# Kernel optimization log

Measured on AMD Instinct MI355X. Metric: run time of the kernel, lower is better.

Reference implementation:

```python
import jax, jax.numpy as jnp
from jax import lax
import numpy as np

STRIDE = 8  # == slice_width
EMBED_DIM = 512


def setup_inputs() -> dict:
    key = jax.random.key(0)
    k0, k1, k2, k3, k4 = jax.random.split(key, 5)
    B, C, H, W = 64, 1, 32, 8192
    images = jax.random.normal(k0, (B, C, H, W), dtype=jnp.float32)
    u = lambda k, s: jax.random.uniform(k, s, jnp.float32, -0.08, 0.08)
    conv_w = u(k1, (1, 1, 3, 3))            # OIHW, 1->1 channel, 3x3
    conv_b = u(k2, (1,))
    lin_w = u(k3, (H * STRIDE, EMBED_DIM))   # bridge: slice_height*slice_width -> embed_dim
    lin_b = u(k4, (EMBED_DIM,))
    return {"images": images, "conv_w": conv_w, "conv_b": conv_b, "lin_w": lin_w, "lin_b": lin_b}


def reference(images, conv_w, conv_b, lin_w, lin_b):
    B, C, H, W = images.shape
    S = W // STRIDE  # src_len (number of width-slices)
    # Windowing: non-overlapping width slices -> a single reshape/transpose
    # [B, C, H, W] -> [B*S, C, H, stride]
    sl = images.reshape(B, C, H, S, STRIDE).transpose(0, 3, 1, 2, 4)
    pixels = sl.reshape(B * S, C, H, STRIDE)
    # Conv2d(1,1,3x3, padding=1) + ReLU (same spatial shape)
    y = lax.conv_general_dilated(
        pixels, conv_w, window_strides=(1, 1), padding="SAME",
        dimension_numbers=("NCHW", "OIHW", "NCHW"))
    y = jax.nn.relu(y + conv_b[None, :, None, None])
    # Bridge linear on flattened slice pixels
    feats = y.reshape(B * S, H * STRIDE)
    emb = feats @ lin_w + lin_b
    return emb.reshape(B, S, EMBED_DIM)
```

## Files before the change

### kernel.cpp

```cpp
#include <hip/hip_runtime.h>
#include <hip/hip_bf16.h>
#include <stdint.h>

#define HEIGHT 32
#define WIDTH  8192
#define KDIM   256
#define NDIM   512
#define NSLICES 65536
#define NMTILES 2048

typedef float f32x4  __attribute__((ext_vector_type(4)));
typedef float f32x16 __attribute__((ext_vector_type(16)));
typedef short bf16x8 __attribute__((ext_vector_type(8)));

__device__ __forceinline__ ushort f2bf(float x) {
  union { float f; uint32_t u; } un; un.f = x;
  uint32_t u = un.u;
  u += 0x7FFFu + ((u >> 16) & 1u);
  return (ushort)(u >> 16);
}

__device__ __forceinline__ void load_row8(float* r, const float* p) {
  f32x4 lo = *reinterpret_cast<const f32x4*>(p);
  f32x4 hi = *reinterpret_cast<const f32x4*>(p + 4);
#pragma unroll
  for (int w = 0; w < 4; ++w) { r[w] = lo[w]; r[4 + w] = hi[w]; }
}

__global__ __launch_bounds__(256) void prep_wt2_kernel(const float* __restrict__ lin_w,
                                                       ushort* __restrict__ wt2) {
  const int idx = blockIdx.x * 256 + threadIdx.x;
  const int ln  = idx & 63;
  const int k0  = (idx >> 6) & 15;
  const int nb  = idx >> 10;
  const int n   = nb * 32 + (ln & 31);
  const int kb  = k0 * 16 + (ln >> 5) * 8;
  bf16x8 p;
#pragma unroll
  for (int e = 0; e < 8; ++e) p[e] = (short)f2bf(lin_w[(size_t)(kb + e) * NDIM + n]);
  *reinterpret_cast<bf16x8*>(wt2 + (size_t)idx * 8) = p;
}

__global__ __launch_bounds__(256) void fused_kernel(
    const float* __restrict__ images, const float* __restrict__ conv_w,
    const float* __restrict__ conv_b, const ushort* __restrict__ wt2,
    const float* __restrict__ lin_b, float* __restrict__ out) {
  __shared__ ushort A[16 * 64 * 8];

  const int tid = threadIdx.x;
  const int blk = blockIdx.x;

  float cw[9];
#pragma unroll
  for (int i = 0; i < 9; ++i) cw[i] = conv_w[i];
  const float cb = conv_b[0];

  {
    const int sl = tid & 31;
    const int q  = tid >> 5;
    const int s  = blk * 32 + sl;
    const int b  = s >> 10;
    const int slb = s & 1023;
    const float* base = images + (size_t)b * (HEIGHT * WIDTH) + (size_t)slb * 8;
    const int h0 = q * 4;

    float pr[8], cu[8], nx[8];
    if (h0 > 0) load_row8(pr, base + (size_t)(h0 - 1) * WIDTH);
    else {
#pragma unroll
      for (int w = 0; w < 8; ++w) pr[w] = 0.f;
    }
    load_row8(cu, base + (size_t)h0 * WIDTH);

#pragma unroll
    for (int i = 0; i < 4; ++i) {
      const int h = h0 + i;
      if (h + 1 < HEIGHT) load_row8(nx, base + (size_t)(h + 1) * WIDTH);
      else {
#pragma unroll
        for (int w = 0; w < 8; ++w) nx[w] = 0.f;
      }
      float y[8];
#pragma unroll
      for (int w = 0; w < 8; ++w) y[w] = cb;
#pragma unroll
      for (int dw = 0; dw < 3; ++dw) {
        const float c0 = cw[dw], c1 = cw[3 + dw], c2 = cw[6 + dw];
#pragma unroll
        for (int w = 0; w < 8; ++w) {
          const int iw = w + dw - 1;
          if (iw >= 0 && iw < 8) {
            y[w] = fmaf(pr[iw], c0, y[w]);
            y[w] = fmaf(cu[iw], c1, y[w]);
            y[w] = fmaf(nx[iw], c2, y[w]);
          }
        }
      }
      bf16x8 pack;
#pragma unroll
      for (int w = 0; w < 8; ++w) pack[w] = (short)f2bf(fmaxf(y[w], 0.f));
      const int ln = ((h & 1) << 5) | sl;
      const int k0 = h >> 1;
      *reinterpret_cast<bf16x8*>(A + ((size_t)k0 * 64 + ln) * 8) = pack;
#pragma unroll
      for (int w = 0; w < 8; ++w) { pr[w] = cu[w]; cu[w] = nx[w]; }
    }
  }
  __syncthreads();

  const int lane = tid & 63;
  const int wv   = tid >> 6;
  const int la   = lane & 31;
  const int lb   = lane >> 5;
  const size_t row0 = (size_t)blk * 32;

  const ushort* abase = A + (size_t)lane * 8;

#pragma unroll
  for (int pass = 0; pass < 2; ++pass) {
    const int nfb = wv * 4 + pass * 2;
    const ushort* bb = wt2 + ((size_t)nfb * 16) * 512 + (size_t)lane * 8;

    f32x16 acc0, acc1;
#pragma unroll
    for (int i = 0; i < 16; ++i) { acc0[i] = 0.f; acc1[i] = 0.f; }

#pragma unroll
    for (int k0 = 0; k0 < 16; ++k0) {
      const bf16x8 af  = *reinterpret_cast<const bf16x8*>(abase + (size_t)k0 * 512);
      const bf16x8 bf0 = *reinterpret_cast<const bf16x8*>(bb + (size_t)k0 * 512);
      const bf16x8 bf1 = *reinterpret_cast<const bf16x8*>(bb + (size_t)(16 + k0) * 512);
      acc0 = __builtin_amdgcn_mfma_f32_32x32x16_bf16(af, bf0, acc0, 0, 0, 0);
      acc1 = __builtin_amdgcn_mfma_f32_32x32x16_bf16(af, bf1, acc1, 0, 0, 0);
    }

#pragma unroll
    for (int nf = 0; nf < 2; ++nf) {
      const int col = (nfb + nf) * 32 + la;
      const float bias = lin_b[col];
      const f32x16& a = nf ? acc1 : acc0;
#pragma unroll
      for (int reg = 0; reg < 16; ++reg) {
        const int rr = (reg & 3) + 8 * (reg >> 2) + 4 * lb;
        out[(row0 + rr) * NDIM + col] = a[reg] + bias;
      }
    }
  }
}

extern "C" void kernel_launch(void* const* d_in, const int* in_sizes, int n_in,
                              void* d_out, int out_size, void* d_ws, size_t ws_size,
                              hipStream_t stream) {
  const float* images = (const float*)d_in[0];
  const float* conv_w = (const float*)d_in[1];
  const float* conv_b = (const float*)d_in[2];
  const float* lin_w  = (const float*)d_in[3];
  const float* lin_b  = (const float*)d_in[4];
  float* out = (float*)d_out;
  ushort* wt2 = (ushort*)d_ws;

  hipLaunchKernelGGL(prep_wt2_kernel, dim3(64), dim3(256), 0, stream, lin_w, wt2);
  hipLaunchKernelGGL(fused_kernel, dim3(NMTILES), dim3(256), 0, stream,
                     images, conv_w, conv_b, wt2, lin_b, out);
}
```

Measured before the change: 55.61 us.

## Stream weight fragments into double-buffered LDS via global_load_lds pipeline

Replaces direct global loads of weight fragments with asynchronous global-to-LDS copies, double-buffered across the K loop, and merges the two N passes into one pass with four accumulators per wave. The aim is to hide global load latency of B behind MFMAs and let each A fragment be read once per k step instead of twice. It adds 32 KB of LDS per block, which may lower occupancy, raises register use with four 16-wide accumulators, and uses hand-placed waitcnts that could be fragile.

```diff
diff --git a/kernel.cpp b/kernel.cpp
--- a/kernel.cpp
+++ b/kernel.cpp
@@ -12,6 +12,11 @@
 typedef float f32x4  __attribute__((ext_vector_type(4)));
 typedef float f32x16 __attribute__((ext_vector_type(16)));
 typedef short bf16x8 __attribute__((ext_vector_type(8)));
+
+#define GLOAD_LDS16(g, l)                                                       \
+  __builtin_amdgcn_global_load_lds(                                             \
+      (const __attribute__((address_space(1))) void*)(g),                       \
+      (__attribute__((address_space(3))) void*)(l), 16, 0, 0)
 
 __device__ __forceinline__ ushort f2bf(float x) {
   union { float f; uint32_t u; } un; un.f = x;
@@ -46,6 +51,7 @@
     const float* __restrict__ conv_b, const ushort* __restrict__ wt2,
     const float* __restrict__ lin_b, float* __restrict__ out) {
   __shared__ ushort A[16 * 64 * 8];
+  __shared__ ushort Bb[2][16][512];
 
   const int tid = threadIdx.x;
   const int blk = blockIdx.x;
@@ -112,38 +118,59 @@
   const int wv   = tid >> 6;
   const int la   = lane & 31;
   const int lb   = lane >> 5;
-  const size_t row0 = (size_t)blk * 32;
+
+  const ushort* bsrc = wt2 + (size_t)lane * 8;
+#define BFRAG_SRC(nf, k) (bsrc + (((wv * 4 + (nf)) * 16 + (k)) * 512))
+
+#pragma unroll
+  for (int nf = 0; nf < 4; ++nf)
+    GLOAD_LDS16(BFRAG_SRC(nf, 0), &Bb[0][wv * 4 + nf][0]);
+
+  f32x16 acc[4];
+#pragma unroll
+  for (int nf = 0; nf < 4; ++nf)
+#pragma unroll
+    for (int i = 0; i < 16; ++i) acc[nf][i] = 0.f;
 
   const ushort* abase = A + (size_t)lane * 8;
 
 #pragma unroll
-  for (int pass = 0; pass < 2; ++pass) {
-    const int nfb = wv * 4 + pass * 2;
-    const ushort* bb = wt2 + ((size_t)nfb * 16) * 512 + (size_t)lane * 8;
-
-    f32x16 acc0, acc1;
+  for (int k0 = 0; k0 < 16; ++k0) {
+    const int cur = k0 & 1;
+    if (k0 < 15) {
+      asm volatile("s_waitcnt lgkmcnt(0)" ::: "memory");
+      __builtin_amdgcn_sched_barrier(0);
+      const int nxt = cur ^ 1;
 #pragma unroll
-    for (int i = 0; i < 16; ++i) { acc0[i] = 0.f; acc1[i] = 0.f; }
-
-#pragma unroll
-    for (int k0 = 0; k0 < 16; ++k0) {
-      const bf16x8 af  = *reinterpret_cast<const bf16x8*>(abase + (size_t)k0 * 512);
-      const bf16x8 bf0 = *reinterpret_cast<const bf16x8*>(bb + (size_t)k0 * 512);
-      const bf16x8 bf1 = *reinterpret_cast<const bf16x8*>(bb + (size_t)(16 + k0) * 512);
-      acc0 = __builtin_amdgcn_mfma_f32_32x32x16_bf16(af, bf0, acc0, 0, 0, 0);
-      acc1 = __builtin_amdgcn_mfma_f32_32x32x16_bf16(af, bf1, acc1, 0, 0, 0);
+      for (int nf = 0; nf < 4; ++nf)
+        GLOAD_LDS16(BFRAG_SRC(nf, k0 + 1), &Bb[nxt][wv * 4 + nf][0]);
+      asm volatile("s_waitcnt vmcnt(4)" ::: "memory");
+      __builtin_amdgcn_sched_barrier(0);
+    } else {
+      asm volatile("s_waitcnt vmcnt(0)" ::: "memory");
+      __builtin_amdgcn_sched_barrier(0);
     }
 
+    const bf16x8 af = *reinterpret_cast<const bf16x8*>(abase + (size_t)k0 * 512);
+    const bf16x8 b0 = *reinterpret_cast<const bf16x8*>(&Bb[cur][wv * 4 + 0][0] + (size_t)lane * 8);
+    const bf16x8 b1 = *reinterpret_cast<const bf16x8*>(&Bb[cur][wv * 4 + 1][0] + (size_t)lane * 8);
+    const bf16x8 b2 = *reinterpret_cast<const bf16x8*>(&Bb[cur][wv * 4 + 2][0] + (size_t)lane * 8);
+    const bf16x8 b3 = *reinterpret_cast<const bf16x8*>(&Bb[cur][wv * 4 + 3][0] + (size_t)lane * 8);
+    acc[0] = __builtin_amdgcn_mfma_f32_32x32x16_bf16(af, b0, acc[0], 0, 0, 0);
+    acc[1] = __builtin_amdgcn_mfma_f32_32x32x16_bf16(af, b1, acc[1], 0, 0, 0);
+    acc[2] = __builtin_amdgcn_mfma_f32_32x32x16_bf16(af, b2, acc[2], 0, 0, 0);
+    acc[3] = __builtin_amdgcn_mfma_f32_32x32x16_bf16(af, b3, acc[3], 0, 0, 0);
+  }
+
+  const size_t row0 = (size_t)blk * 32;
 #pragma unroll
-    for (int nf = 0; nf < 2; ++nf) {
-      const int col = (nfb + nf) * 32 + la;
-      const float bias = lin_b[col];
-      const f32x16& a = nf ? acc1 : acc0;
+  for (int nf = 0; nf < 4; ++nf) {
+    const int col = wv * 128 + nf * 32 + la;
+    const float bias = lin_b[col];
 #pragma unroll
-      for (int reg = 0; reg < 16; ++reg) {
-        const int rr = (reg & 3) + 8 * (reg >> 2) + 4 * lb;
-        out[(row0 + rr) * NDIM + col] = a[reg] + bias;
-      }
+    for (int reg = 0; reg < 16; ++reg) {
+      const int rr = (reg & 3) + 8 * (reg >> 2) + 4 * lb;
+      out[(row0 + rr) * NDIM + col] = acc[nf][reg] + bias;
     }
   }
 }
```

After: 57.20 us. 2.9% more time.

## Split fused conv+GEMM into separate conv and register-resident-weight GEMM kernels

Applied to the files above, without the earlier changes.

Splits the fused kernel in two. A conv kernel writes bf16 features in MFMA-ready layout to workspace, and a GEMM kernel keeps a 32-column weight fragment in registers while looping over 8 row tiles. This lets each weight fragment be reused across many rows instead of reloading it per block. The cost is an extra global round trip of 32 MB of bf16 features plus a second launch, and the new path runs only when the workspace is large enough.

```diff
diff --git a/kernel.cpp b/kernel.cpp
--- a/kernel.cpp
+++ b/kernel.cpp
@@ -8,6 +8,8 @@
 #define NDIM   512
 #define NSLICES 65536
 #define NMTILES 2048
+#define WT_BYTES (NDIM * KDIM * 2)
+#define FEATS_BYTES ((size_t)NSLICES * KDIM * 2)
 
 typedef float f32x4  __attribute__((ext_vector_type(4)));
 typedef float f32x16 __attribute__((ext_vector_type(16)));
@@ -41,12 +43,119 @@
   *reinterpret_cast<bf16x8*>(wt2 + (size_t)idx * 8) = p;
 }
 
+__global__ __launch_bounds__(256) void conv_kernel(
+    const float* __restrict__ images, const float* __restrict__ conv_w,
+    const float* __restrict__ conv_b, ushort* __restrict__ feats2) {
+  const int blk = blockIdx.x;
+  const int tid = threadIdx.x;
+
+  float cw[9];
+#pragma unroll
+  for (int i = 0; i < 9; ++i) cw[i] = conv_w[i];
+  const float cb = conv_b[0];
+
+  const int sl = tid & 31;
+  const int q  = tid >> 5;
+  const int s  = blk * 32 + sl;
+  const int b  = s >> 10;
+  const int slb = s & 1023;
+  const float* base = images + (size_t)b * (HEIGHT * WIDTH) + (size_t)slb * 8;
+  const int h0 = q * 4;
+
+  float pr[8], cu[8], nx[8];
+  if (h0 > 0) load_row8(pr, base + (size_t)(h0 - 1) * WIDTH);
+  else {
+#pragma unroll
+    for (int w = 0; w < 8; ++w) pr[w] = 0.f;
+  }
+  load_row8(cu, base + (size_t)h0 * WIDTH);
+
+#pragma unroll
+  for (int i = 0; i < 4; ++i) {
+    const int h = h0 + i;
+    if (h + 1 < HEIGHT) load_row8(nx, base + (size_t)(h + 1) * WIDTH);
+    else {
+#pragma unroll
+      for (int w = 0; w < 8; ++w) nx[w] = 0.f;
+    }
+    float y[8];
+#pragma unroll
+    for (int w = 0; w < 8; ++w) y[w] = cb;
+#pragma unroll
+    for (int dw = 0; dw < 3; ++dw) {
+      const float c0 = cw[dw], c1 = cw[3 + dw], c2 = cw[6 + dw];
+#pragma unroll
+      for (int w = 0; w < 8; ++w) {
+        const int iw = w + dw - 1;
+        if (iw >= 0 && iw < 8) {
+          y[w] = fmaf(pr[iw], c0, y[w]);
+          y[w] = fmaf(cu[iw], c1, y[w]);
+          y[w] = fmaf(nx[iw], c2, y[w]);
+        }
+      }
+    }
+    bf16x8 pack;
+#pragma unroll
+    for (int w = 0; w < 8; ++w) pack[w] = (short)f2bf(fmaxf(y[w], 0.f));
+    const int ln = ((h & 1) << 5) | sl;
+    const int k0 = h >> 1;
+    *reinterpret_cast<bf16x8*>(feats2 + (((size_t)blk * 16 + k0) * 64 + ln) * 8) = pack;
+#pragma unroll
+    for (int w = 0; w < 8; ++w) { pr[w] = cu[w]; cu[w] = nx[w]; }
+  }
+}
+
+__global__ __launch_bounds__(512) void gemm2_kernel(
+    const ushort* __restrict__ feats2, const ushort* __restrict__ wt2,
+    const float* __restrict__ lin_b, float* __restrict__ out) {
+  const int tid  = threadIdx.x;
+  const int lane = tid & 63;
+  const int wv   = tid >> 6;
+  const int blk  = blockIdx.x;
+  const int m0   = (blk & 255) * 8;
+  const int nb   = ((blk >> 8) << 3) | wv;
+  const int la   = lane & 31;
+  const int lb   = lane >> 5;
+
+  bf16x8 Bf[16];
+  {
+    const ushort* bb = wt2 + ((size_t)nb * 16) * 512 + (size_t)lane * 8;
+#pragma unroll
+    for (int k0 = 0; k0 < 16; ++k0)
+      Bf[k0] = *reinterpret_cast<const bf16x8*>(bb + (size_t)k0 * 512);
+  }
+
+  const int col = nb * 32 + la;
+  const float bias = lin_b[col];
+
+  for (int mi = 0; mi < 8; ++mi) {
+    const int m = m0 + mi;
+    const ushort* ab = feats2 + ((size_t)m * 16) * 512 + (size_t)lane * 8;
+
+    f32x16 acc;
+#pragma unroll
+    for (int i = 0; i < 16; ++i) acc[i] = bias;
+
+#pragma unroll
+    for (int k0 = 0; k0 < 16; ++k0) {
+      const bf16x8 af = *reinterpret_cast<const bf16x8*>(ab + (size_t)k0 * 512);
+      acc = __builtin_amdgcn_mfma_f32_32x32x16_bf16(af, Bf[k0], acc, 0, 0, 0);
+    }
+
+    const size_t row0 = (size_t)m * 32;
+#pragma unroll
+    for (int reg = 0; reg < 16; ++reg) {
+      const int rr = (reg & 3) + 8 * (reg >> 2) + 4 * lb;
+      out[(row0 + rr) * NDIM + col] = acc[reg];
+    }
+  }
+}
+
 __global__ __launch_bounds__(256) void fused_kernel(
     const float* __restrict__ images, const float* __restrict__ conv_w,
     const float* __restrict__ conv_b, const ushort* __restrict__ wt2,
     const float* __restrict__ lin_b, float* __restrict__ out) {
   __shared__ ushort A[16 * 64 * 8];
-
   const int tid = threadIdx.x;
   const int blk = blockIdx.x;
 
@@ -113,7 +222,6 @@
   const int la   = lane & 31;
   const int lb   = lane >> 5;
   const size_t row0 = (size_t)blk * 32;
-
   const ushort* abase = A + (size_t)lane * 8;
 
 #pragma unroll
@@ -160,6 +268,15 @@
   ushort* wt2 = (ushort*)d_ws;
 
   hipLaunchKernelGGL(prep_wt2_kernel, dim3(64), dim3(256), 0, stream, lin_w, wt2);
-  hipLaunchKernelGGL(fused_kernel, dim3(NMTILES), dim3(256), 0, stream,
-                     images, conv_w, conv_b, wt2, lin_b, out);
-}
+
+  if (ws_size >= (size_t)WT_BYTES + FEATS_BYTES) {
+    ushort* feats2 = (ushort*)((char*)d_ws + WT_BYTES);
+    hipLaunchKernelGGL(conv_kernel, dim3(NMTILES), dim3(256), 0, stream,
+                       images, conv_w, conv_b, feats2);
+    hipLaunchKernelGGL(gemm2_kernel, dim3(512), dim3(512), 0, stream,
+                       feats2, wt2, lin_b, out);
+  } else {
+    hipLaunchKernelGGL(fused_kernel, dim3(NMTILES), dim3(256), 0, stream,
+                       images, conv_w, conv_b, wt2, lin_b, out);
+  }
+}
```

Result: slower. 66.91 us (+20.3%).
